# Kernel tuning notes

Hardware: AMD Instinct MI355X
Metric: run time of the kernel (lower is better)

## Reference

```python
import jax, jax.numpy as jnp
import numpy as np

DIM = 768
HEADS = 12
E = 8
TOPK = 2
EPS = 1e-5


def layer_norm(x, g, b):
    m = jnp.mean(x, axis=-1, keepdims=True)
    v = jnp.mean((x - m) ** 2, axis=-1, keepdims=True)
    return (x - m) * jax.lax.rsqrt(v + EPS) * g + b


def setup_inputs() -> dict:
    key = jax.random.key(0)
    ks = jax.random.split(key, 12)
    B, N, C = 16, 1024, DIM
    s = 0.02
    return {
        "x": jax.random.normal(ks[0], (B, N, C), jnp.float32),
        "noise": jax.random.normal(ks[1], (B, N, E), jnp.float32),
        "ln1_g": jnp.ones((C,), jnp.float32),
        "ln1_b": jnp.zeros((C,), jnp.float32),
        "qkv_w": jax.random.normal(ks[2], (C, 3 * C), jnp.float32) * s,  # pre-transposed
        "proj_w": jax.random.normal(ks[3], (C, C), jnp.float32) * s,
        "proj_b": jnp.zeros((C,), jnp.float32),
        "ln2_g": jnp.ones((C,), jnp.float32),
        "ln2_b": jnp.zeros((C,), jnp.float32),
        "route_w": jax.random.normal(ks[4], (C, E), jnp.float32) * s,
        "route_b": jnp.zeros((E,), jnp.float32),
        "rln_g": jnp.ones((E,), jnp.float32),
        "rln_b": jnp.zeros((E,), jnp.float32),
        "expert_w": jax.random.normal(ks[5], (E, C, C), jnp.float32) * s,  # [E, in, out]
        "expert_b": jnp.zeros((E, C), jnp.float32),
    }


def reference(x, noise, ln1_g, ln1_b, qkv_w, proj_w, proj_b, ln2_g, ln2_b,
              route_w, route_b, rln_g, rln_b, expert_w, expert_b):
    B, N, C = x.shape
    H = HEADS
    Dh = C // H
    scale = Dh ** -0.5

    # --- Attention branch ---
    h = layer_norm(x, ln1_g, ln1_b)
    qkv = (h @ qkv_w).reshape(B, N, 3, H, Dh)
    q, k, v = qkv[:, :, 0], qkv[:, :, 1], qkv[:, :, 2]  # [B,N,H,Dh]
    attn = jnp.einsum('bnhd,bmhd->bhnm', q, k) * scale
    attn = jax.nn.softmax(attn, axis=-1)
    o = jnp.einsum('bhnm,bmhd->bnhd', attn, v).reshape(B, N, C)
    x = x + o @ proj_w + proj_b

    # --- MoE branch ---
    h = layer_norm(x, ln2_g, ln2_b)
    logits = layer_norm(h @ route_w + route_b, rln_g, rln_b)  # [B,N,E]
    rw = jax.nn.softmax(logits, axis=-1) + noise * (1.0 / E)
    topk_w, topk_idx = jax.lax.top_k(rw, TOPK)               # [B,N,K]
    topk_w = jax.nn.softmax(topk_w, axis=-1)

    # dense all-expert compute (faithful to source): [B,N,E,C]
    expert_out = jnp.einsum('bnc,ecd->bned', h, expert_w) + expert_b
    selected = jnp.take_along_axis(expert_out, topk_idx[..., None], axis=2)  # [B,N,K,C]
    moe = jnp.sum(selected * topk_w[..., None], axis=2)
    return x + moe
```

## Files before the change

### kernel.cpp

```cpp
#include <hip/hip_runtime.h>

typedef unsigned short u16;
typedef unsigned int u32;
typedef _Float16 f16;
typedef short bf16x8 __attribute__((ext_vector_type(8)));
typedef f16 f16x8 __attribute__((ext_vector_type(8)));
typedef float f32x4 __attribute__((ext_vector_type(4)));
typedef u32 u32x4 __attribute__((ext_vector_type(4)));

#define TOKENS 16384
#define CDIM 768
#define NEXP 8

__device__ __forceinline__ float b2f(u16 u) {
  return __uint_as_float(((u32)u) << 16);
}
__device__ __forceinline__ u16 f2b(float f) {
  u32 u = __float_as_uint(f);
  return (u16)((u + 0x7fffu + ((u >> 16) & 1u)) >> 16);
}
__device__ __forceinline__ f32x4 mfma_bf(bf16x8 a, bf16x8 b, f32x4 c) {
  return __builtin_amdgcn_mfma_f32_16x16x32_bf16(a, b, c, 0, 0, 0);
}
__device__ __forceinline__ f32x4 mfma_h(f16x8 a, f16x8 b, f32x4 c) {
  return __builtin_amdgcn_mfma_f32_16x16x32_f16(a, b, c, 0, 0, 0);
}
__device__ __forceinline__ void split8(const float* v, f16x8& h, f16x8& l) {
#pragma unroll
  for (int i = 0; i < 8; i++) {
    const f16 hh = (f16)v[i];
    h[i] = hh;
    l[i] = (f16)(v[i] - (float)hh);
  }
}

__global__ __launch_bounds__(256) void transpose_split_f16(
    const float* __restrict__ in, f16* __restrict__ oh, f16* __restrict__ ol,
    int K, int N) {
  __shared__ float tile[64][65];
  const int n0 = blockIdx.x * 64, k0 = blockIdx.y * 64;
#pragma unroll
  for (int i = 0; i < 16; i++) {
    const int s = threadIdx.x + i * 256;
    const int r = s >> 6, c = s & 63;
    tile[r][c] = in[(size_t)(k0 + r) * N + n0 + c];
  }
  __syncthreads();
#pragma unroll
  for (int i = 0; i < 16; i++) {
    const int s = threadIdx.x + i * 256;
    const int r = s >> 6, c = s & 63;
    const float v = tile[c][r];
    const f16 h = (f16)v;
    oh[(size_t)(n0 + r) * K + k0 + c] = h;
    ol[(size_t)(n0 + r) * K + k0 + c] = (f16)(v - (float)h);
  }
}

__global__ __launch_bounds__(256) void transpose_f32_bf16(
    const float* __restrict__ in, u16* __restrict__ out, int K, int N) {
  __shared__ u16 tile[64][65];
  const int z = blockIdx.z;
  in += (size_t)z * K * N;
  out += (size_t)z * K * N;
  const int n0 = blockIdx.x * 64, k0 = blockIdx.y * 64;
#pragma unroll
  for (int i = 0; i < 16; i++) {
    const int s = threadIdx.x + i * 256;
    const int r = s >> 6, c = s & 63;
    tile[r][c] = f2b(in[(size_t)(k0 + r) * N + n0 + c]);
  }
  __syncthreads();
#pragma unroll
  for (int i = 0; i < 16; i++) {
    const int s = threadIdx.x + i * 256;
    const int r = s >> 6, c = s & 63;
    out[(size_t)(n0 + r) * K + k0 + c] = tile[c][r];
  }
}

template <bool BF16OUT>
__global__ __launch_bounds__(256) void ln_rows(const float* __restrict__ in,
                                               const float* __restrict__ g,
                                               const float* __restrict__ bt,
                                               void* __restrict__ out) {
  const int row = blockIdx.x * 4 + (threadIdx.x >> 6);
  const int lane = threadIdx.x & 63;
  const size_t base = (size_t)row * CDIM;
  float v[12];
  float s = 0.f, ss = 0.f;
#pragma unroll
  for (int j = 0; j < 12; j++) {
    const int idx = lane + j * 64;
    v[j] = in[base + idx];
    s += v[j];
    ss += v[j] * v[j];
  }
#pragma unroll
  for (int m = 1; m < 64; m <<= 1) {
    s += __shfl_xor(s, m);
    ss += __shfl_xor(ss, m);
  }
  const float mean = s * (1.f / CDIM);
  const float var = ss * (1.f / CDIM) - mean * mean;
  const float rs = rsqrtf(var + 1e-5f);
#pragma unroll
  for (int j = 0; j < 12; j++) {
    const int idx = lane + j * 64;
    const float y = (v[j] - mean) * rs * g[idx] + bt[idx];
    if (BF16OUT)
      ((u16*)out)[base + idx] = f2b(y);
    else
      ((float*)out)[base + idx] = y;
  }
}

template <int EPI>
__global__ __launch_bounds__(256) void gemm_f16s(
    const float* __restrict__ A, const f16* __restrict__ Bth,
    const f16* __restrict__ Btl, float* __restrict__ C, int M, int N, int K,
    const float* __restrict__ bias, const float* __restrict__ xres) {
  __shared__ f16 Ah[128 * 64];
  __shared__ f16 Al[128 * 64];
  __shared__ f16 Bh[128 * 64];
  __shared__ f16 Bl[128 * 64];
  const int tid = threadIdx.x;
  const int lane = tid & 63, wv = tid >> 6;
  const int wr = wv >> 1, wc = wv & 1;
  const int lm = lane & 15, lq = lane >> 4;
  const int m0 = blockIdx.y * 128, n0 = blockIdx.x * 128;
  f32x4 acc[4][4];
  const f32x4 z4 = {0.f, 0.f, 0.f, 0.f};
#pragma unroll
  for (int i = 0; i < 4; i++)
#pragma unroll
    for (int j = 0; j < 4; j++) acc[i][j] = z4;

  for (int k0 = 0; k0 < K; k0 += 64) {
    __syncthreads();
#pragma unroll
    for (int i = 0; i < 4; i++) {
      const int s = tid + i * 256;
      const int r = s >> 3, g = s & 7;
      float av[8];
      *(float4*)&av[0] = *(const float4*)(A + (size_t)(m0 + r) * K + k0 + g * 8);
      *(float4*)&av[4] =
          *(const float4*)(A + (size_t)(m0 + r) * K + k0 + g * 8 + 4);
      f16x8 hh, ll;
      split8(av, hh, ll);
      const int sw = r * 64 + ((g ^ (r & 7)) << 3);
      *(f16x8*)(&Ah[sw]) = hh;
      *(f16x8*)(&Al[sw]) = ll;
      *(f16x8*)(&Bh[sw]) = *(const f16x8*)(Bth + (size_t)(n0 + r) * K + k0 + g * 8);
      *(f16x8*)(&Bl[sw]) = *(const f16x8*)(Btl + (size_t)(n0 + r) * K + k0 + g * 8);
    }
    __syncthreads();
#pragma unroll
    for (int kx = 0; kx < 8; kx += 4) {
      f16x8 afh[4], afl[4], bfh[4], bfl[4];
#pragma unroll
      for (int i = 0; i < 4; i++) {
        const int ra = wr * 64 + i * 16 + lm;
        const int aw = ra * 64 + (((ra & 7) ^ (kx + lq)) << 3);
        afh[i] = *(const f16x8*)(&Ah[aw]);
        afl[i] = *(const f16x8*)(&Al[aw]);
        const int rb = wc * 64 + i * 16 + lm;
        const int bw = rb * 64 + (((rb & 7) ^ (kx + lq)) << 3);
        bfh[i] = *(const f16x8*)(&Bh[bw]);
        bfl[i] = *(const f16x8*)(&Bl[bw]);
      }
#pragma unroll
      for (int i = 0; i < 4; i++)
#pragma unroll
        for (int j = 0; j < 4; j++) {
          acc[i][j] = mfma_h(afh[i], bfh[j], acc[i][j]);
          acc[i][j] = mfma_h(afh[i], bfl[j], acc[i][j]);
          acc[i][j] = mfma_h(afl[i], bfh[j], acc[i][j]);
        }
    }
  }
#pragma unroll
  for (int i = 0; i < 4; i++)
#pragma unroll
    for (int r = 0; r < 4; r++) {
      const size_t row = m0 + wr * 64 + i * 16 + lq * 4 + r;
#pragma unroll
      for (int j = 0; j < 4; j++) {
        const int col = n0 + wc * 64 + j * 16 + lm;
        float v = acc[i][j][r];
        if (EPI == 1) v += bias[col] + xres[row * N + col];
        C[row * N + col] = v;
      }
    }
}

__global__ __launch_bounds__(256) void attn_f16s(const float* __restrict__ qkvf,
                                                 float* __restrict__ o,
                                                 int qb) {
  __shared__ f16 Kh[64 * 64];
  __shared__ f16 Kl[64 * 64];
  __shared__ f16 Vh[64 * 64];
  __shared__ f16 Vl[64 * 64];
  __shared__ f16 Ph[4 * 16 * 64];
  __shared__ f16 Pl[4 * 16 * 64];
  const int bz = blockIdx.z, h = blockIdx.y, qt = blockIdx.x;
  const int tid = threadIdx.x, wv = tid >> 6, lane = tid & 63;
  const int lm = lane & 15, lq = lane >> 4;

  f16x8 qh[2], ql[2];
  {
    const size_t qbase =
        (size_t)(bz * 1024 + qt * 64 + wv * 16 + lm) * 2304 + h * 64;
#pragma unroll
    for (int f = 0; f < 2; f++) {
      float v[8];
      *(float4*)&v[0] = *(const float4*)(qkvf + qbase + f * 32 + lq * 8);
      *(float4*)&v[4] = *(const float4*)(qkvf + qbase + f * 32 + lq * 8 + 4);
      split8(v, qh[f], ql[f]);
    }
  }
  const f32x4 z4 = {0.f, 0.f, 0.f, 0.f};
  f32x4 oacc[4];
#pragma unroll
  for (int jb = 0; jb < 4; jb++) oacc[jb] = z4;
  float mrun[4], lrun[4];
#pragma unroll
  for (int r = 0; r < 4; r++) {
    mrun[r] = -1e30f;
    lrun[r] = 0.f;
  }
  const int vd = tid & 63;
  const int vkg = tid >> 6;
  f16* pwh = &Ph[wv * 16 * 64];
  f16* pwl = &Pl[wv * 16 * 64];

  for (int kt = 0; kt < 16; kt++) {
    __syncthreads();
#pragma unroll
    for (int i = 0; i < 2; i++) {
      const int s2 = tid + i * 256;
      const int r = s2 >> 3, g = s2 & 7;
      const size_t kb =
          (size_t)(bz * 1024 + kt * 64 + r) * 2304 + 768 + h * 64 + g * 8;
      float v[8];
      *(float4*)&v[0] = *(const float4*)(qkvf + kb);
      *(float4*)&v[4] = *(const float4*)(qkvf + kb + 4);
      f16x8 hh, ll;
      split8(v, hh, ll);
      const int sw = r * 64 + ((g ^ (r & 7)) << 3);
      *(f16x8*)(&Kh[sw]) = hh;
      *(f16x8*)(&Kl[sw]) = ll;
    }
#pragma unroll
    for (int sseg = 0; sseg < 2; sseg++) {
      const int k0v = vkg * 16 + sseg * 8;
      float v[8];
#pragma unroll
      for (int j = 0; j < 8; j++)
        v[j] = qkvf[(size_t)(bz * 1024 + kt * 64 + k0v + j) * 2304 + 1536 +
                    h * 64 + vd];
      f16x8 hh, ll;
      split8(v, hh, ll);
      const int g = k0v >> 3;
      const int sw = vd * 64 + ((g ^ (vd & 7)) << 3);
      *(f16x8*)(&Vh[sw]) = hh;
      *(f16x8*)(&Vl[sw]) = ll;
    }
    __syncthreads();

    f32x4 sa[4];
#pragma unroll
    for (int j = 0; j < 4; j++) sa[j] = z4;
#pragma unroll
    for (int kx = 0; kx < 8; kx += 4) {
      const f16x8 ah = qh[kx >> 2], al = ql[kx >> 2];
#pragma unroll
      for (int j = 0; j < 4; j++) {
        const int rb = j * 16 + lm;
        const int bw = rb * 64 + (((rb & 7) ^ (kx + lq)) << 3);
        const f16x8 bh = *(const f16x8*)(&Kh[bw]);
        const f16x8 bl = *(const f16x8*)(&Kl[bw]);
        sa[j] = mfma_h(ah, bh, sa[j]);
        sa[j] = mfma_h(ah, bl, sa[j]);
        sa[j] = mfma_h(al, bh, sa[j]);
      }
    }
#pragma unroll
    for (int j = 0; j < 4; j++)
#pragma unroll
      for (int r = 0; r < 4; r++) sa[j][r] *= 0.125f;

#pragma unroll
    for (int r = 0; r < 4; r++) {
      float mx = fmaxf(fmaxf(sa[0][r], sa[1][r]), fmaxf(sa[2][r], sa[3][r]));
      mx = fmaxf(mx, __shfl_xor(mx, 1));
      mx = fmaxf(mx, __shfl_xor(mx, 2));
      mx = fmaxf(mx, __shfl_xor(mx, 4));
      mx = fmaxf(mx, __shfl_xor(mx, 8));
      const float mnew = fmaxf(mrun[r], mx);
      const float alpha = expf(mrun[r] - mnew);
      float ps = 0.f;
#pragma unroll
      for (int j = 0; j < 4; j++) {
        const float p = expf(sa[j][r] - mnew);
        sa[j][r] = p;
        ps += p;
      }
      ps += __shfl_xor(ps, 1);
      ps += __shfl_xor(ps, 2);
      ps += __shfl_xor(ps, 4);
      ps += __shfl_xor(ps, 8);
      lrun[r] = lrun[r] * alpha + ps;
      mrun[r] = mnew;
#pragma unroll
      for (int jb = 0; jb < 4; jb++) oacc[jb][r] *= alpha;
    }

#pragma unroll
    for (int j = 0; j < 4; j++)
#pragma unroll
      for (int r = 0; r < 4; r++) {
        const int qr = lq * 4 + r;
        const int key = j * 16 + lm;
        const int ad = qr * 64 + (((qr & 7) ^ (key >> 3)) << 3) + (key & 7);
        const float p = sa[j][r];
        const f16 ph = (f16)p;
        pwh[ad] = ph;
        pwl[ad] = (f16)(p - (float)ph);
      }
#pragma unroll
    for (int kx2 = 0; kx2 < 8; kx2 += 4) {
      const int pw = lm * 64 + (((lm & 7) ^ (kx2 + lq)) << 3);
      const f16x8 pah = *(const f16x8*)(&pwh[pw]);
      const f16x8 pal = *(const f16x8*)(&pwl[pw]);
#pragma unroll
      for (int jb = 0; jb < 4; jb++) {
        const int rb = jb * 16 + lm;
        const int vw = rb * 64 + (((rb & 7) ^ (kx2 + lq)) << 3);
        const f16x8 vh = *(const f16x8*)(&Vh[vw]);
        const f16x8 vl = *(const f16x8*)(&Vl[vw]);
        oacc[jb] = mfma_h(pah, vh, oacc[jb]);
        oacc[jb] = mfma_h(pah, vl, oacc[jb]);
        oacc[jb] = mfma_h(pal, vh, oacc[jb]);
      }
    }
  }
  const int gtok = (qb * 4 + bz) * 1024 + qt * 64;
#pragma unroll
  for (int r = 0; r < 4; r++) {
    const float inv = 1.f / lrun[r];
    const size_t row = (size_t)gtok + wv * 16 + lq * 4 + r;
#pragma unroll
    for (int jb = 0; jb < 4; jb++) {
      const int col = h * 64 + jb * 16 + lm;
      o[row * CDIM + col] = oacc[jb][r] * inv;
    }
  }
}

__global__ __launch_bounds__(256) void gemm_expert(
    const u16* __restrict__ A, const u16* __restrict__ Bt,
    float* __restrict__ C, int N, int K, const float* __restrict__ bias,
    const int* __restrict__ counts, const int* __restrict__ tokList,
    const float* __restrict__ wgtList) {
  __shared__ u16 As[128 * 64];
  __shared__ u16 Bs[128 * 64];
  const int tid = threadIdx.x;
  const int lane = tid & 63, wv = tid >> 6;
  const int wr = wv >> 1, wc = wv & 1;
  const int lm = lane & 15, lq = lane >> 4;
  const int m0 = blockIdx.y * 128, n0 = blockIdx.x * 128;
  const int e = blockIdx.z;
  const int cnt = counts[e];
  if (m0 >= cnt) return;
  const u16* Bte = Bt + (size_t)e * N * K;
  const int* tokl = tokList + e * TOKENS;
  const float* wl = wgtList + e * TOKENS;
  const float* biasE = bias + e * N;
  f32x4 acc[4][4];
  const f32x4 z4 = {0.f, 0.f, 0.f, 0.f};
#pragma unroll
  for (int i = 0; i < 4; i++)
#pragma unroll
    for (int j = 0; j < 4; j++) acc[i][j] = z4;

  for (int k0 = 0; k0 < K; k0 += 64) {
    __syncthreads();
#pragma unroll
    for (int i = 0; i < 4; i++) {
      const int s = tid + i * 256;
      const int r = s >> 3, g = s & 7;
      u32x4 av;
      const int row = m0 + r;
      if (row < cnt) {
        av = *(const u32x4*)(A + (size_t)tokl[row] * K + k0 + g * 8);
      } else {
        av = (u32x4){0u, 0u, 0u, 0u};
      }
      *(u32x4*)(&As[r * 64 + ((g ^ (r & 7)) << 3)]) = av;
      const u32x4 bv = *(const u32x4*)(Bte + (size_t)(n0 + r) * K + k0 + g * 8);
      *(u32x4*)(&Bs[r * 64 + ((g ^ (r & 7)) << 3)]) = bv;
    }
    __syncthreads();
#pragma unroll
    for (int kx = 0; kx < 8; kx += 4) {
      bf16x8 af[4], bfv[4];
#pragma unroll
      for (int i = 0; i < 4; i++) {
        const int ra = wr * 64 + i * 16 + lm;
        af[i] = *(const bf16x8*)(&As[ra * 64 + (((ra & 7) ^ (kx + lq)) << 3)]);
        const int rb = wc * 64 + i * 16 + lm;
        bfv[i] = *(const bf16x8*)(&Bs[rb * 64 + (((rb & 7) ^ (kx + lq)) << 3)]);
      }
#pragma unroll
      for (int i = 0; i < 4; i++)
#pragma unroll
        for (int j = 0; j < 4; j++)
          acc[i][j] = mfma_bf(af[i], bfv[j], acc[i][j]);
    }
  }
#pragma unroll
  for (int i = 0; i < 4; i++)
#pragma unroll
    for (int r = 0; r < 4; r++) {
      const int rowi = m0 + wr * 64 + i * 16 + lq * 4 + r;
      if (rowi < cnt) {
        const int tok = tokl[rowi];
        const float w = wl[rowi];
#pragma unroll
        for (int j = 0; j < 4; j++) {
          const int col = n0 + wc * 64 + j * 16 + lm;
          atomicAdd(&C[(size_t)tok * N + col], (acc[i][j][r] + biasE[col]) * w);
        }
      }
    }
}

__global__ __launch_bounds__(256) void router_kernel(
    const float* __restrict__ x2, const float* __restrict__ g2,
    const float* __restrict__ b2, const float* __restrict__ rw,
    const float* __restrict__ rb, const float* __restrict__ rlng,
    const float* __restrict__ rlnb, const float* __restrict__ noise,
    int* __restrict__ eidx, float* __restrict__ ewgt) {
  const int token = blockIdx.x * 4 + (threadIdx.x >> 6);
  const int lane = threadIdx.x & 63;
  const size_t base = (size_t)token * CDIM;
  float v[12];
  float s = 0.f, ss = 0.f;
#pragma unroll
  for (int j = 0; j < 12; j++) {
    const int idx = lane + j * 64;
    v[j] = x2[base + idx];
    s += v[j];
    ss += v[j] * v[j];
  }
#pragma unroll
  for (int m = 1; m < 64; m <<= 1) {
    s += __shfl_xor(s, m);
    ss += __shfl_xor(ss, m);
  }
  const float mean = s * (1.f / CDIM);
  const float var = ss * (1.f / CDIM) - mean * mean;
  const float rs = rsqrtf(var + 1e-5f);

  float acc[8];
#pragma unroll
  for (int e = 0; e < 8; e++) acc[e] = 0.f;
#pragma unroll
  for (int j = 0; j < 12; j++) {
    const int d = lane + j * 64;
    const float hv = (v[j] - mean) * rs * g2[d] + b2[d];
    const f32x4 w0v = *(const f32x4*)(rw + (size_t)d * 8);
    const f32x4 w1v = *(const f32x4*)(rw + (size_t)d * 8 + 4);
#pragma unroll
    for (int e = 0; e < 4; e++) {
      acc[e] += hv * w0v[e];
      acc[e + 4] += hv * w1v[e];
    }
  }
#pragma unroll
  for (int m = 1; m < 64; m <<= 1)
#pragma unroll
    for (int e = 0; e < 8; e++) acc[e] += __shfl_xor(acc[e], m);

  float y[8];
  float emean = 0.f;
#pragma unroll
  for (int e = 0; e < 8; e++) {
    y[e] = acc[e] + rb[e];
    emean += y[e];
  }
  emean *= 0.125f;
  float evar = 0.f;
#pragma unroll
  for (int e = 0; e < 8; e++) {
    const float d = y[e] - emean;
    evar += d * d;
  }
  evar *= 0.125f;
  const float ers = rsqrtf(evar + 1e-5f);
  float lg[8];
  float mx = -1e30f;
#pragma unroll
  for (int e = 0; e < 8; e++) {
    lg[e] = (y[e] - emean) * ers * rlng[e] + rlnb[e];
    mx = fmaxf(mx, lg[e]);
  }
  float se = 0.f;
#pragma unroll
  for (int e = 0; e < 8; e++) {
    lg[e] = expf(lg[e] - mx);
    se += lg[e];
  }
  const float inv = 1.f / se;
  float r2[8];
#pragma unroll
  for (int e = 0; e < 8; e++)
    r2[e] = lg[e] * inv + noise[(size_t)token * 8 + e] * 0.125f;

  int e0 = 0;
  float v0 = r2[0];
#pragma unroll
  for (int e = 1; e < 8; e++)
    if (r2[e] > v0) {
      v0 = r2[e];
      e0 = e;
    }
  int e1 = -1;
  float v1 = -1e30f;
#pragma unroll
  for (int e = 0; e < 8; e++)
    if (e != e0 && r2[e] > v1) {
      v1 = r2[e];
      e1 = e;
    }
  const float w0 = 1.f / (1.f + expf(v1 - v0));
  if (lane == 0) {
    eidx[token * 2] = e0;
    eidx[token * 2 + 1] = e1;
    ewgt[token * 2] = w0;
    ewgt[token * 2 + 1] = 1.f - w0;
  }
}

__global__ __launch_bounds__(256) void build_lists(
    const int* __restrict__ eidx, const float* __restrict__ ewgt,
    int* __restrict__ counts, int* __restrict__ tokL,
    float* __restrict__ wgtL) {
  const int e = blockIdx.x;
  __shared__ int cnt;
  if (threadIdx.x == 0) cnt = 0;
  __syncthreads();
  const int lane = threadIdx.x & 63;
  for (int t = threadIdx.x; t < TOKENS; t += 256) {
#pragma unroll
    for (int k = 0; k < 2; k++) {
      const bool match = (eidx[t * 2 + k] == e);
      const unsigned long long mb = __ballot(match);
      if (mb) {
        const int leader = __ffsll((unsigned long long)mb) - 1;
        int base = 0;
        if (lane == leader) base = atomicAdd(&cnt, __popcll(mb));
        base = __shfl(base, leader);
        if (match) {
          const int rank = __popcll(mb & ((1ull << lane) - 1ull));
          tokL[e * TOKENS + base + rank] = t;
          wgtL[e * TOKENS + base + rank] = ewgt[t * 2 + k];
        }
      }
    }
  }
  __syncthreads();
  if (threadIdx.x == 0) counts[e] = cnt;
}

__global__ __launch_bounds__(256) void copy_f32(const float* __restrict__ in,
                                                float* __restrict__ out) {
  const int i = (blockIdx.x * 256 + threadIdx.x) * 4;
  *(float4*)(out + i) = *(const float4*)(in + i);
}

extern "C" void kernel_launch(void* const* d_in, const int* in_sizes, int n_in,
                              void* d_out, int out_size, void* d_ws,
                              size_t ws_size, hipStream_t stream) {
  const float* x = (const float*)d_in[0];
  const float* noise = (const float*)d_in[1];
  const float* ln1_g = (const float*)d_in[2];
  const float* ln1_b = (const float*)d_in[3];
  const float* qkv_w = (const float*)d_in[4];
  const float* proj_w = (const float*)d_in[5];
  const float* proj_b = (const float*)d_in[6];
  const float* ln2_g = (const float*)d_in[7];
  const float* ln2_b = (const float*)d_in[8];
  const float* route_w = (const float*)d_in[9];
  const float* route_b = (const float*)d_in[10];
  const float* rln_g = (const float*)d_in[11];
  const float* rln_b = (const float*)d_in[12];
  const float* expert_w = (const float*)d_in[13];
  const float* expert_b = (const float*)d_in[14];

  char* ws = (char*)d_ws;
  float* x2f = (float*)(ws);
  float* qkvf = (float*)(ws + 50331648);
  u16* exp_wt = (u16*)(ws + 50331648);
  u16* h2 = (u16*)(ws + 59768832);
  int* counts = (int*)(ws + 84934656);
  int* eidx = (int*)(ws + 84934912);
  float* ewgt = (float*)(ws + 85065984);
  int* tokL = (int*)(ws + 85197056);
  float* wgtL = (float*)(ws + 85721344);
  f16* qkvw_h = (f16*)(ws + 88080384);
  f16* qkvw_l = (f16*)(ws + 91619328);
  f16* projw_h = (f16*)(ws + 95158272);
  f16* projw_l = (f16*)(ws + 96337920);
  float* h1f = (float*)d_out;

  const dim3 blk(256);
  transpose_split_f16<<<dim3(36, 12), blk, 0, stream>>>(qkv_w, qkvw_h, qkvw_l,
                                                        768, 2304);
  transpose_split_f16<<<dim3(12, 12), blk, 0, stream>>>(proj_w, projw_h,
                                                        projw_l, 768, 768);
  ln_rows<false><<<dim3(4096), blk, 0, stream>>>(x, ln1_g, ln1_b, h1f);
  for (int q = 0; q < 4; q++) {
    gemm_f16s<0><<<dim3(18, 32), blk, 0, stream>>>(
        h1f + (size_t)q * 4096 * 768, qkvw_h, qkvw_l, qkvf, 4096, 2304, 768,
        nullptr, nullptr);
    attn_f16s<<<dim3(16, 12, 4), blk, 0, stream>>>(qkvf, h1f, q);
  }
  gemm_f16s<1><<<dim3(6, 128), blk, 0, stream>>>(h1f, projw_h, projw_l, x2f,
                                                 16384, 768, 768, proj_b, x);
  ln_rows<true><<<dim3(4096), blk, 0, stream>>>(x2f, ln2_g, ln2_b, h2);
  transpose_f32_bf16<<<dim3(12, 12, 8), blk, 0, stream>>>(expert_w, exp_wt,
                                                          768, 768);
  router_kernel<<<dim3(4096), blk, 0, stream>>>(x2f, ln2_g, ln2_b, route_w,
                                                route_b, rln_g, rln_b, noise,
                                                eidx, ewgt);
  build_lists<<<dim3(8), blk, 0, stream>>>(eidx, ewgt, counts, tokL, wgtL);
  gemm_expert<<<dim3(6, 128, 8), blk, 0, stream>>>(
      h2, exp_wt, x2f, 768, 768, expert_b, counts, tokL, wgtL);
  copy_f32<<<dim3(12288), blk, 0, stream>>>(x2f, (float*)d_out);
}
```

Baseline: 1.199 ms.

## Prefetch next K-tile into registers in routed expert GEMM

```diff
diff --git a/kernel.cpp b/kernel.cpp
--- a/kernel.cpp
+++ b/kernel.cpp
@@ -377,6 +377,19 @@
   const int* tokl = tokList + e * TOKENS;
   const float* wl = wgtList + e * TOKENS;
   const float* biasE = bias + e * N;
+
+  const int r0 = tid >> 3, g = tid & 7;
+  const int swz = (g ^ (r0 & 7)) << 3;
+  const u16* ap[4];
+  const u16* bp[4];
+#pragma unroll
+  for (int i = 0; i < 4; i++) {
+    const int row = m0 + r0 + i * 32;
+    const int tok = (row < cnt) ? tokl[row] : 0;
+    ap[i] = A + (size_t)tok * K + g * 8;
+    bp[i] = Bte + (size_t)(n0 + r0 + i * 32) * K + g * 8;
+  }
+
   f32x4 acc[4][4];
   const f32x4 z4 = {0.f, 0.f, 0.f, 0.f};
 #pragma unroll
@@ -384,24 +397,28 @@
 #pragma unroll
     for (int j = 0; j < 4; j++) acc[i][j] = z4;
 
+  u32x4 pa[4], pb[4];
+#pragma unroll
+  for (int i = 0; i < 4; i++) {
+    pa[i] = *(const u32x4*)(ap[i]);
+    pb[i] = *(const u32x4*)(bp[i]);
+  }
+#pragma unroll
+  for (int i = 0; i < 4; i++) {
+    *(u32x4*)(&As[(r0 + i * 32) * 64 + swz]) = pa[i];
+    *(u32x4*)(&Bs[(r0 + i * 32) * 64 + swz]) = pb[i];
+  }
+
   for (int k0 = 0; k0 < K; k0 += 64) {
     __syncthreads();
-#pragma unroll
-    for (int i = 0; i < 4; i++) {
-      const int s = tid + i * 256;
-      const int r = s >> 3, g = s & 7;
-      u32x4 av;
-      const int row = m0 + r;
-      if (row < cnt) {
-        av = *(const u32x4*)(A + (size_t)tokl[row] * K + k0 + g * 8);
-      } else {
-        av = (u32x4){0u, 0u, 0u, 0u};
-      }
-      *(u32x4*)(&As[r * 64 + ((g ^ (r & 7)) << 3)]) = av;
-      const u32x4 bv = *(const u32x4*)(Bte + (size_t)(n0 + r) * K + k0 + g * 8);
-      *(u32x4*)(&Bs[r * 64 + ((g ^ (r & 7)) << 3)]) = bv;
-    }
-    __syncthreads();
+    const bool more = (k0 + 64) < K;
+    if (more) {
+#pragma unroll
+      for (int i = 0; i < 4; i++) {
+        pa[i] = *(const u32x4*)(ap[i] + k0 + 64);
+        pb[i] = *(const u32x4*)(bp[i] + k0 + 64);
+      }
+    }
 #pragma unroll
     for (int kx = 0; kx < 8; kx += 4) {
       bf16x8 af[4], bfv[4];
@@ -417,6 +434,14 @@
 #pragma unroll
         for (int j = 0; j < 4; j++)
           acc[i][j] = mfma_bf(af[i], bfv[j], acc[i][j]);
+    }
+    __syncthreads();
+    if (more) {
+#pragma unroll
+      for (int i = 0; i < 4; i++) {
+        *(u32x4*)(&As[(r0 + i * 32) * 64 + swz]) = pa[i];
+        *(u32x4*)(&Bs[(r0 + i * 32) * 64 + swz]) = pb[i];
+      }
     }
   }
 #pragma unroll
```

Result: no change. 1.183 ms (-1.3%).
